# Optimization experiments

Measured on AMD Instinct MI355X. Metric: run time of the kernel, lower is better.

Reference implementation:

```python
import jax, jax.numpy as jnp
import numpy as np

B, D_IN, H1, H2, LAT, K = 32768, 512, 256, 128, 64, 2048
BN_EPS = 1e-5
COMMIT = 0.25


def _linear_w(k, i, o):
    # xavier-uniform-ish init
    lim = np.sqrt(6.0 / (i + o)).astype(np.float32)
    return jax.random.uniform(k, (i, o), jnp.float32, -lim, lim)


def _bn_params(keys, n):
    g = jax.random.uniform(keys[0], (n,), jnp.float32, 0.5, 1.5)
    b = 0.1 * jax.random.normal(keys[1], (n,), jnp.float32)
    m = 0.1 * jax.random.normal(keys[2], (n,), jnp.float32)
    v = jax.random.uniform(keys[3], (n,), jnp.float32, 0.5, 1.5)
    return g, b, m, v


def setup_inputs() -> dict:
    key = jax.random.key(0)
    ks = jax.random.split(key, 32)
    inp = {"x": jax.random.normal(ks[0], (B, D_IN), jnp.float32)}
    # encoder: 512 -> 256 -> 128 -> 64
    inp["ew1"], inp["eb1"] = _linear_w(ks[1], D_IN, H1), jnp.zeros((H1,), jnp.float32)
    inp["eg1"], inp["ebt1"], inp["em1"], inp["ev1"] = _bn_params(jax.random.split(ks[2], 4), H1)
    inp["ew2"], inp["eb2"] = _linear_w(ks[3], H1, H2), jnp.zeros((H2,), jnp.float32)
    inp["eg2"], inp["ebt2"], inp["em2"], inp["ev2"] = _bn_params(jax.random.split(ks[4], 4), H2)
    inp["ew3"], inp["eb3"] = _linear_w(ks[5], H2, LAT), jnp.zeros((LAT,), jnp.float32)
    # codebook (num_embeddings, latent_dim)
    inp["codebook"] = _linear_w(ks[6], K, LAT).reshape(K, LAT)
    # decoder: 64 -> 128 -> 256 -> 512
    inp["dw1"], inp["db1"] = _linear_w(ks[7], LAT, H2), jnp.zeros((H2,), jnp.float32)
    inp["dg1"], inp["dbt1"], inp["dm1"], inp["dv1"] = _bn_params(jax.random.split(ks[8], 4), H2)
    inp["dw2"], inp["db2"] = _linear_w(ks[9], H2, H1), jnp.zeros((H1,), jnp.float32)
    inp["dg2"], inp["dbt2"], inp["dm2"], inp["dv2"] = _bn_params(jax.random.split(ks[10], 4), H1)
    inp["dw3"], inp["db3"] = _linear_w(ks[11], H1, D_IN), jnp.zeros((D_IN,), jnp.float32)
    return inp


def _bn(x, g, b, m, v):
    # BatchNorm1d in eval mode: running stats
    return (x - m) * (g * jax.lax.rsqrt(v + BN_EPS)) + b


def reference(x, ew1, eb1, eg1, ebt1, em1, ev1,
              ew2, eb2, eg2, ebt2, em2, ev2,
              ew3, eb3, codebook,
              dw1, db1, dg1, dbt1, dm1, dv1,
              dw2, db2, dg2, dbt2, dm2, dv2,
              dw3, db3):
    # ---- encoder MLP (Dropout is identity in eval) ----
    h = _bn(jax.nn.relu(x @ ew1 + eb1), eg1, ebt1, em1, ev1)
    h = _bn(jax.nn.relu(h @ ew2 + eb2), eg2, ebt2, em2, ev2)
    z_e = h @ ew3 + eb3  # [B, LAT]

    # ---- vector quantization: cdist + argmin + gather ----
    # squared L2 distance (argmin-equivalent to cdist p=2)
    d2 = (jnp.sum(z_e * z_e, axis=1, keepdims=True)
          + jnp.sum(codebook * codebook, axis=1)[None, :]
          - 2.0 * (z_e @ codebook.T))  # [B, K]
    idx = jnp.argmin(d2, axis=-1)  # [B]
    z_q = codebook[idx]  # gather, [B, LAT]

    codebook_loss = jnp.mean((z_q - jax.lax.stop_gradient(z_e)) ** 2)
    commit_loss = jnp.mean((z_e - jax.lax.stop_gradient(z_q)) ** 2)
    vq_loss = codebook_loss + COMMIT * commit_loss

    # straight-through estimator
    z_q = z_e + jax.lax.stop_gradient(z_q - z_e)

    # ---- decoder MLP ----
    h = _bn(jax.nn.relu(z_q @ dw1 + db1), dg1, dbt1, dm1, dv1)
    h = _bn(jax.nn.relu(h @ dw2 + db2), dg2, dbt2, dm2, dv2)
    x_recon = h @ dw3 + db3  # [B, D_IN]

    recon_err = jnp.mean((x_recon - x) ** 2)
    return x_recon, vq_loss, idx, recon_err
```

## Files before the change

kernel.cpp:

```cpp
#include <hip/hip_runtime.h>

#define B_ROWS 32768
#define D_IN   512
#define H1_N   256
#define H2_N   128
#define LAT_N  64
#define K_CB   2048

#define VQ_MARGIN 6.0e-3f

typedef __attribute__((ext_vector_type(8))) short s8v;
typedef __attribute__((ext_vector_type(4))) float f4v;

__device__ inline unsigned short f2bf(float f) {
    union { float f; unsigned u; } v; v.f = f;
    unsigned r = v.u + 0x7fffu + ((v.u >> 16) & 1u);
    return (unsigned short)(r >> 16);
}
__device__ inline float bf2f(unsigned short h) {
    union { unsigned u; float f; } v; v.u = ((unsigned)h) << 16;
    return v.f;
}

template <int MODE, int K, int CT, bool ASPLIT>
__global__ __launch_bounds__(256, 2) void mfma_gemm(
    const float* __restrict__ A_f32,
    const unsigned short* __restrict__ A_hi,
    const unsigned short* __restrict__ A_lo,
    const unsigned short* __restrict__ w_hi,
    const unsigned short* __restrict__ w_lo,
    const float* __restrict__ bias,
    const float* __restrict__ bn_g, const float* __restrict__ bn_b,
    const float* __restrict__ bn_m, const float* __restrict__ bn_v,
    unsigned short* __restrict__ out_hi, unsigned short* __restrict__ out_lo,
    float* __restrict__ out_f32,
    const float* __restrict__ xref, float* __restrict__ partials, int N)
{
    const int lane = threadIdx.x & 63;
    const int wv = threadIdx.x >> 6;
    const int wr = wv >> 1, wc = wv & 1;
    const int rbase = blockIdx.x * 128 + wr * 64;
    const int cbase = blockIdx.y * (32 * CT) + wc * (16 * CT);
    const int lr = lane & 15, lg = lane >> 4;

    f4v acc[4][CT];
#pragma unroll
    for (int rt = 0; rt < 4; ++rt)
#pragma unroll
        for (int ct = 0; ct < CT; ++ct)
            acc[rt][ct] = (f4v){0.f, 0.f, 0.f, 0.f};

    for (int ks = 0; ks < K / 32; ++ks) {
        s8v ah[4], al[4], bh[CT], bl[CT];
#pragma unroll
        for (int rt = 0; rt < 4; ++rt) {
            size_t off = (size_t)(rbase + rt * 16 + lr) * K + ks * 32 + lg * 8;
            if constexpr (ASPLIT) {
                const float* p = &A_f32[off];
                float4 v0 = *reinterpret_cast<const float4*>(p);
                float4 v1 = *reinterpret_cast<const float4*>(p + 4);
                float fv[8] = {v0.x, v0.y, v0.z, v0.w, v1.x, v1.y, v1.z, v1.w};
                unsigned uu[8], llv[8];
#pragma unroll
                for (int j = 0; j < 8; ++j) {
                    uu[j] = __float_as_uint(fv[j]);
                    float lo = fv[j] - __uint_as_float(uu[j] & 0xffff0000u);
                    llv[j] = __float_as_uint(lo);
                }
                union { s8v v; unsigned w[4]; } H, L;
#pragma unroll
                for (int m = 0; m < 4; ++m) {
                    H.w[m] = __builtin_amdgcn_perm(uu[2 * m + 1], uu[2 * m], 0x07060302u);
                    L.w[m] = __builtin_amdgcn_perm(llv[2 * m + 1], llv[2 * m], 0x07060302u);
                }
                ah[rt] = H.v;
                al[rt] = L.v;
            } else {
                ah[rt] = *reinterpret_cast<const s8v*>(&A_hi[off]);
                al[rt] = *reinterpret_cast<const s8v*>(&A_lo[off]);
            }
        }
#pragma unroll
        for (int ct = 0; ct < CT; ++ct) {
            size_t off = (size_t)(cbase + ct * 16 + lr) * K + ks * 32 + lg * 8;
            bh[ct] = *reinterpret_cast<const s8v*>(&w_hi[off]);
            bl[ct] = *reinterpret_cast<const s8v*>(&w_lo[off]);
        }
#pragma unroll
        for (int rt = 0; rt < 4; ++rt)
#pragma unroll
            for (int ct = 0; ct < CT; ++ct) {
                acc[rt][ct] = __builtin_amdgcn_mfma_f32_16x16x32_bf16(
                    ah[rt], bh[ct], acc[rt][ct], 0, 0, 0);
                acc[rt][ct] = __builtin_amdgcn_mfma_f32_16x16x32_bf16(
                    al[rt], bh[ct], acc[rt][ct], 0, 0, 0);
                acc[rt][ct] = __builtin_amdgcn_mfma_f32_16x16x32_bf16(
                    ah[rt], bl[ct], acc[rt][ct], 0, 0, 0);
            }
    }

    float sq = 0.f;
#pragma unroll
    for (int ct = 0; ct < CT; ++ct) {
        int col = cbase + ct * 16 + lr;
        float bi = bias[col];
        float sc = 0.f, sh = 0.f;
        if (MODE == 0) {
            float s = bn_g[col] * rsqrtf(bn_v[col] + 1e-5f);
            sc = s;
            sh = bn_b[col] - bn_m[col] * s;
        }
#pragma unroll
        for (int rt = 0; rt < 4; ++rt)
#pragma unroll
            for (int i = 0; i < 4; ++i) {
                int row = rbase + rt * 16 + lg * 4 + i;
                float v = acc[rt][ct][i] + bi;
                if (MODE == 0) v = fmaxf(v, 0.f) * sc + sh;
                if (MODE == 0 || MODE == 3) {
                    unsigned u = __float_as_uint(v);
                    out_hi[(size_t)row * N + col] = (unsigned short)(u >> 16);
                    out_lo[(size_t)row * N + col] =
                        f2bf(v - __uint_as_float(u & 0xffff0000u));
                }
                if (MODE == 2) {
                    float d = v - xref[(size_t)row * N + col];
                    sq = fmaf(d, d, sq);
                }
                if (MODE == 2 || MODE == 3)
                    out_f32[(size_t)row * N + col] = v;
            }
    }
    if (MODE == 2) {
        __shared__ float red[256];
        red[threadIdx.x] = sq;
        __syncthreads();
        for (int off = 128; off > 0; off >>= 1) {
            if (threadIdx.x < off) red[threadIdx.x] += red[threadIdx.x + off];
            __syncthreads();
        }
        if (threadIdx.x == 0)
            partials[blockIdx.y * gridDim.x + blockIdx.x] = red[0];
    }
}

__device__ inline void wprep_body(const float* __restrict__ w,
                                  unsigned short* __restrict__ w_hi,
                                  unsigned short* __restrict__ w_lo,
                                  int K, int N, int idx)
{
    if (idx >= N * K) return;
    int n = idx / K, k = idx - n * K;
    float f = w[(size_t)k * N + n];
    unsigned u = __float_as_uint(f);
    float lo = f - __uint_as_float(u & 0xffff0000u);
    w_hi[idx] = (unsigned short)(u >> 16);
    w_lo[idx] = f2bf(lo);
}

__global__ __launch_bounds__(256) void prep_all(
    const float* __restrict__ dw3, unsigned short* w3hi, unsigned short* w3lo,
    const float* __restrict__ dw2, unsigned short* w2hi, unsigned short* w2lo,
    const float* __restrict__ dw1, unsigned short* w1hi, unsigned short* w1lo,
    const float* __restrict__ ew1, unsigned short* e1hi, unsigned short* e1lo,
    const float* __restrict__ ew2, unsigned short* e2hi, unsigned short* e2lo,
    const float* __restrict__ ew3, unsigned short* e3hi, unsigned short* e3lo,
    const float* __restrict__ cb, unsigned short* cb_hi, unsigned short* cb_lo,
    float* __restrict__ cn, int* __restrict__ rcnt, float* __restrict__ repairp)
{
    int bid = blockIdx.x;
    int tid = threadIdx.x;
    if (bid < 512) {
        wprep_body(dw3, w3hi, w3lo, H1_N, D_IN, bid * 256 + tid);
    } else if (bid < 640) {
        wprep_body(dw2, w2hi, w2lo, H2_N, H1_N, (bid - 512) * 256 + tid);
    } else if (bid < 672) {
        wprep_body(dw1, w1hi, w1lo, LAT_N, H2_N, (bid - 640) * 256 + tid);
    } else if (bid < 1184) {
        wprep_body(ew1, e1hi, e1lo, D_IN, H1_N, (bid - 672) * 256 + tid);
    } else if (bid < 1312) {
        wprep_body(ew2, e2hi, e2lo, H1_N, H2_N, (bid - 1184) * 256 + tid);
    } else if (bid < 1344) {
        wprep_body(ew3, e3hi, e3lo, H2_N, LAT_N, (bid - 1312) * 256 + tid);
    } else {
        int blk = bid - 1344;
        if (blk == 0) {
            if (tid == 0) rcnt[0] = 0;
            repairp[tid] = 0.f;
        }
        int j = blk * 256 + tid;
        float s = 0.f;
#pragma unroll
        for (int lq = 0; lq < 16; ++lq) {
            float4 v = *reinterpret_cast<const float4*>(&cb[(size_t)j * LAT_N + lq * 4]);
            float e[4] = {v.x, v.y, v.z, v.w};
            ushort4 h, l;
            unsigned short* hp = &h.x;
            unsigned short* lp = &l.x;
#pragma unroll
            for (int t = 0; t < 4; ++t) {
                s = fmaf(e[t], e[t], s);
                unsigned short hb = f2bf(e[t]);
                hp[t] = hb;
                lp[t] = f2bf(e[t] - bf2f(hb));
            }
            *reinterpret_cast<ushort4*>(&cb_hi[(size_t)j * LAT_N + lq * 4]) = h;
            *reinterpret_cast<ushort4*>(&cb_lo[(size_t)j * LAT_N + lq * 4]) = l;
        }
        cn[j] = s;
    }
}

__global__ __launch_bounds__(256) void vq_mfma(
    const unsigned short* __restrict__ zhi, const unsigned short* __restrict__ zlo,
    const unsigned short* __restrict__ cb_hi,
    const unsigned short* __restrict__ cb_lo, const float* __restrict__ cnorm,
    float4* __restrict__ cand)
{
    const int lane = threadIdx.x & 63;
    const int wid  = blockIdx.x * 4 + (threadIdx.x >> 6);
    const int rbase = (wid >> 3) * 64;
    const int cblk  = wid & 7;
    const int cbase = cblk * 256;
    const int lr = lane & 15;
    const int lg = lane >> 4;

    s8v a_hi[4][2], a_lo[4][2];
#pragma unroll
    for (int rt = 0; rt < 4; ++rt) {
        int row = rbase + rt * 16 + lr;
#pragma unroll
        for (int ks = 0; ks < 2; ++ks) {
            size_t off = (size_t)row * LAT_N + ks * 32 + lg * 8;
            a_hi[rt][ks] = *reinterpret_cast<const s8v*>(&zhi[off]);
            a_lo[rt][ks] = *reinterpret_cast<const s8v*>(&zlo[off]);
        }
    }

    float b1[4][4], b2[4][4];
    int j1[4][4];
#pragma unroll
    for (int rt = 0; rt < 4; ++rt)
#pragma unroll
        for (int i = 0; i < 4; ++i) {
            b1[rt][i] = 3.4e38f; b2[rt][i] = 3.4e38f; j1[rt][i] = 0;
        }

    for (int ct = 0; ct < 16; ++ct) {
        int col = cbase + ct * 16 + lr;
        const unsigned short* ph = &cb_hi[(size_t)col * LAT_N + lg * 8];
        const unsigned short* pl = &cb_lo[(size_t)col * LAT_N + lg * 8];
        s8v bh0 = *reinterpret_cast<const s8v*>(ph);
        s8v bh1 = *reinterpret_cast<const s8v*>(ph + 32);
        s8v bl0 = *reinterpret_cast<const s8v*>(pl);
        s8v bl1 = *reinterpret_cast<const s8v*>(pl + 32);
        float cn = cnorm[col];
#pragma unroll
        for (int rt = 0; rt < 4; ++rt) {
            f4v acc = {0.f, 0.f, 0.f, 0.f};
            acc = __builtin_amdgcn_mfma_f32_16x16x32_bf16(a_hi[rt][0], bh0, acc, 0, 0, 0);
            acc = __builtin_amdgcn_mfma_f32_16x16x32_bf16(a_hi[rt][1], bh1, acc, 0, 0, 0);
            acc = __builtin_amdgcn_mfma_f32_16x16x32_bf16(a_lo[rt][0], bh0, acc, 0, 0, 0);
            acc = __builtin_amdgcn_mfma_f32_16x16x32_bf16(a_lo[rt][1], bh1, acc, 0, 0, 0);
            acc = __builtin_amdgcn_mfma_f32_16x16x32_bf16(a_hi[rt][0], bl0, acc, 0, 0, 0);
            acc = __builtin_amdgcn_mfma_f32_16x16x32_bf16(a_hi[rt][1], bl1, acc, 0, 0, 0);
#pragma unroll
            for (int i = 0; i < 4; ++i) {
                float d = fmaf(-2.f, acc[i], cn);
                if (d < b1[rt][i]) {
                    b2[rt][i] = b1[rt][i];
                    b1[rt][i] = d;
                    j1[rt][i] = col;
                } else if (d < b2[rt][i]) {
                    b2[rt][i] = d;
                }
            }
        }
    }

#pragma unroll
    for (int off = 1; off < 16; off <<= 1) {
#pragma unroll
        for (int rt = 0; rt < 4; ++rt)
#pragma unroll
            for (int i = 0; i < 4; ++i) {
                float o1 = __shfl_xor(b1[rt][i], off);
                float o2 = __shfl_xor(b2[rt][i], off);
                int oj = __shfl_xor(j1[rt][i], off);
                float nb2 = fminf(fmaxf(b1[rt][i], o1), fminf(b2[rt][i], o2));
                if (o1 < b1[rt][i] ||
                    (o1 == b1[rt][i] && oj < j1[rt][i])) {
                    b1[rt][i] = o1;
                    j1[rt][i] = oj;
                }
                b2[rt][i] = nb2;
            }
    }
    if (lr == 0) {
#pragma unroll
        for (int rt = 0; rt < 4; ++rt)
#pragma unroll
            for (int i = 0; i < 4; ++i) {
                int row = rbase + rt * 16 + lg * 4 + i;
                cand[(size_t)row * 8 + cblk] = make_float4(
                    b1[rt][i], __int_as_float(j1[rt][i]), b2[rt][i], 0.f);
            }
    }
}

__global__ __launch_bounds__(256) void vq_merge(
    const float4* __restrict__ cand, const float* __restrict__ z,
    const float* __restrict__ cb,
    const unsigned short* __restrict__ cbhi,
    const unsigned short* __restrict__ cblo,
    unsigned short* __restrict__ zqhi, unsigned short* __restrict__ zqlo,
    float* __restrict__ idxf,
    int* __restrict__ rlist, int* __restrict__ rcnt,
    float* __restrict__ mergep)
{
    __shared__ float red[256];
    int tid = threadIdx.x;
    int row = blockIdx.x * 256 + tid;
    const float4* c = &cand[(size_t)row * 8];
    float4 c0 = c[0];
    float b1 = c0.x, b2 = c0.z;
    int j1 = __float_as_int(c0.y);
#pragma unroll
    for (int t = 1; t < 8; ++t) {
        float4 ct = c[t];
        float o1 = ct.x, o2 = ct.z;
        int oj = __float_as_int(ct.y);
        float nb2 = fminf(fmaxf(b1, o1), fminf(b2, o2));
        if (o1 < b1 || (o1 == b1 && oj < j1)) { b1 = o1; j1 = oj; }
        b2 = nb2;
    }
    idxf[row] = (float)j1;
    float sq = 0.f;
    if (b2 - b1 >= VQ_MARGIN) {
#pragma unroll
        for (int lq = 0; lq < 16; ++lq) {
            float4 cv = *reinterpret_cast<const float4*>(&cb[(size_t)j1 * LAT_N + lq * 4]);
            float4 zv = *reinterpret_cast<const float4*>(&z[(size_t)row * LAT_N + lq * 4]);
            float d0 = cv.x - zv.x, d1 = cv.y - zv.y;
            float d2 = cv.z - zv.z, d3 = cv.w - zv.w;
            sq = fmaf(d0, d0, sq); sq = fmaf(d1, d1, sq);
            sq = fmaf(d2, d2, sq); sq = fmaf(d3, d3, sq);
        }
        const uint4* gh = reinterpret_cast<const uint4*>(&cbhi[(size_t)j1 * LAT_N]);
        const uint4* gl = reinterpret_cast<const uint4*>(&cblo[(size_t)j1 * LAT_N]);
        uint4* dh = reinterpret_cast<uint4*>(&zqhi[(size_t)row * LAT_N]);
        uint4* dl = reinterpret_cast<uint4*>(&zqlo[(size_t)row * LAT_N]);
#pragma unroll
        for (int q = 0; q < 8; ++q) { dh[q] = gh[q]; dl[q] = gl[q]; }
    } else {
        int s = atomicAdd(rcnt, 1);
        if (s < B_ROWS) rlist[s] = row;
    }
    red[tid] = sq;
    __syncthreads();
    for (int off = 128; off > 0; off >>= 1) {
        if (tid < off) red[tid] += red[tid + off];
        __syncthreads();
    }
    if (tid == 0) mergep[blockIdx.x] = red[0];
}

#define RB 8
__global__ __launch_bounds__(256) void vq_repair(
    const int* __restrict__ rcnt, const int* __restrict__ rlist,
    const float* __restrict__ x,
    const float* __restrict__ ew1, const float* __restrict__ eb1,
    const float* __restrict__ eg1, const float* __restrict__ ebt1,
    const float* __restrict__ em1, const float* __restrict__ ev1,
    const float* __restrict__ ew2, const float* __restrict__ eb2,
    const float* __restrict__ eg2, const float* __restrict__ ebt2,
    const float* __restrict__ em2, const float* __restrict__ ev2,
    const float* __restrict__ ew3, const float* __restrict__ eb3,
    const float* __restrict__ cb, const float* __restrict__ cn,
    const unsigned short* __restrict__ cbhi,
    const unsigned short* __restrict__ cblo,
    unsigned short* __restrict__ zqhi, unsigned short* __restrict__ zqlo,
    float* __restrict__ idxf, float* __restrict__ repairp)
{
    __shared__ float sx[RB][D_IN];
    __shared__ float sh1[RB][H1_N];
    __shared__ float sh2[RB][H2_N];
    __shared__ float sz[RB][LAT_N];
    __shared__ float rv[256];
    __shared__ int ri[256];
    const int tid = threadIdx.x;
    const int count = min(rcnt[0], B_ROWS);
    if (blockIdx.x * RB >= count) return;
    float lsum = 0.f;
    for (int base = blockIdx.x * RB; base < count; base += gridDim.x * RB) {
        int nr = min(RB, count - base);
        __syncthreads();
        for (int s = tid; s < nr * (D_IN / 4); s += 256) {
            int r = s / (D_IN / 4), q = s - r * (D_IN / 4);
            int rr = rlist[base + r];
            rr = ((unsigned)rr < (unsigned)B_ROWS) ? rr : 0;
            *reinterpret_cast<float4*>(&sx[r][q * 4]) =
                *reinterpret_cast<const float4*>(&x[(size_t)rr * D_IN + q * 4]);
        }
        __syncthreads();
        {
            float a[RB];
#pragma unroll
            for (int r = 0; r < RB; ++r) a[r] = 0.f;
            for (int k = 0; k < D_IN; ++k) {
                float w = ew1[(size_t)k * H1_N + tid];
#pragma unroll
                for (int r = 0; r < RB; ++r) a[r] = fmaf(sx[r][k], w, a[r]);
            }
            float s1 = eg1[tid] * rsqrtf(ev1[tid] + 1e-5f);
            float t1 = ebt1[tid] - em1[tid] * s1;
            float bv = eb1[tid];
#pragma unroll
            for (int r = 0; r < RB; ++r) {
                float h = fmaxf(a[r] + bv, 0.f);
                sh1[r][tid] = h * s1 + t1;
            }
        }
        __syncthreads();
        {
            int c = tid & 127, rg = (tid >> 7) * 4;
            float a[4] = {0.f, 0.f, 0.f, 0.f};
            for (int k = 0; k < H1_N; ++k) {
                float w = ew2[(size_t)k * H2_N + c];
#pragma unroll
                for (int r = 0; r < 4; ++r) a[r] = fmaf(sh1[rg + r][k], w, a[r]);
            }
            float s2 = eg2[c] * rsqrtf(ev2[c] + 1e-5f);
            float t2 = ebt2[c] - em2[c] * s2;
            float bv = eb2[c];
#pragma unroll
            for (int r = 0; r < 4; ++r) {
                float h = fmaxf(a[r] + bv, 0.f);
                sh2[rg + r][c] = h * s2 + t2;
            }
        }
        __syncthreads();
        {
            int c = tid & 63, rg = (tid >> 6) * 2;
            float a0 = 0.f, a1 = 0.f;
            for (int k = 0; k < H2_N; ++k) {
                float w = ew3[(size_t)k * LAT_N + c];
                a0 = fmaf(sh2[rg][k], w, a0);
                a1 = fmaf(sh2[rg + 1][k], w, a1);
            }
            sz[rg][c] = a0 + eb3[c];
            sz[rg + 1][c] = a1 + eb3[c];
        }
        __syncthreads();
        float bv[RB];
        int bj[RB];
#pragma unroll
        for (int r = 0; r < RB; ++r) { bv[r] = 3.4e38f; bj[r] = 0; }
        for (int k = 0; k < K_CB / 256; ++k) {
            int cidx = tid + k * 256;
            float a[RB];
#pragma unroll
            for (int r = 0; r < RB; ++r) a[r] = 0.f;
            const float* cp = &cb[(size_t)cidx * LAT_N];
#pragma unroll 2
            for (int d4 = 0; d4 < 16; ++d4) {
                float4 cv = *reinterpret_cast<const float4*>(cp + d4 * 4);
#pragma unroll
                for (int r = 0; r < RB; ++r) {
                    a[r] = fmaf(sz[r][d4 * 4 + 0], cv.x, a[r]);
                    a[r] = fmaf(sz[r][d4 * 4 + 1], cv.y, a[r]);
                    a[r] = fmaf(sz[r][d4 * 4 + 2], cv.z, a[r]);
                    a[r] = fmaf(sz[r][d4 * 4 + 3], cv.w, a[r]);
                }
            }
            float cnv = cn[cidx];
#pragma unroll
            for (int r = 0; r < RB; ++r) {
                float d = fmaf(-2.f, a[r], cnv);
                if (d < bv[r] || (d == bv[r] && cidx < bj[r])) {
                    bv[r] = d; bj[r] = cidx;
                }
            }
        }
        for (int r = 0; r < RB; ++r) {
            if (r >= nr) break;
            rv[tid] = bv[r];
            ri[tid] = bj[r];
            __syncthreads();
            for (int off = 128; off > 0; off >>= 1) {
                if (tid < off) {
                    float ov = rv[tid + off];
                    int oi = ri[tid + off];
                    if (ov < rv[tid] || (ov == rv[tid] && oi < ri[tid])) {
                        rv[tid] = ov; ri[tid] = oi;
                    }
                }
                __syncthreads();
            }
            int bjf = ri[0];
            int rr = rlist[base + r];
            bool ok = (unsigned)rr < (unsigned)B_ROWS;
            rr = ok ? rr : 0;
            if (tid == 0 && ok) idxf[rr] = (float)bjf;
            float v = 0.f;
            if (tid < 64) {
                float d = cb[(size_t)bjf * LAT_N + tid] - sz[r][tid];
                v = d * d;
            }
            __syncthreads();
            rv[tid] = v;
            __syncthreads();
            for (int off = 128; off > 0; off >>= 1) {
                if (tid < off) rv[tid] += rv[tid + off];
                __syncthreads();
            }
            if (tid == 0) lsum += rv[0];
            if (ok) {
                if (tid < 8)
                    reinterpret_cast<uint4*>(&zqhi[(size_t)rr * LAT_N])[tid] =
                        reinterpret_cast<const uint4*>(&cbhi[(size_t)bjf * LAT_N])[tid];
                else if (tid < 16)
                    reinterpret_cast<uint4*>(&zqlo[(size_t)rr * LAT_N])[tid - 8] =
                        reinterpret_cast<const uint4*>(&cblo[(size_t)bjf * LAT_N])[tid - 8];
            }
            __syncthreads();
        }
    }
    if (tid == 0) repairp[blockIdx.x] = lsum;
}

__global__ __launch_bounds__(256) void finalize_kernel(
    const float* __restrict__ mergep, int nm,
    const float* __restrict__ repairp, int nr,
    const float* __restrict__ rep, int nre,
    float* __restrict__ vq_out, float* __restrict__ re_out)
{
    __shared__ float s[256];
    int tid = threadIdx.x;
    float a = 0.f;
    for (int i = tid; i < nm; i += 256) a += mergep[i];
    for (int i = tid; i < nr; i += 256) a += repairp[i];
    s[tid] = a;
    __syncthreads();
    for (int off = 128; off > 0; off >>= 1) {
        if (tid < off) s[tid] += s[tid + off];
        __syncthreads();
    }
    if (tid == 0) *vq_out = 1.25f * s[0] / (float)(B_ROWS * LAT_N);
    __syncthreads();
    float b = 0.f;
    for (int i = tid; i < nre; i += 256) b += rep[i];
    s[tid] = b;
    __syncthreads();
    for (int off = 128; off > 0; off >>= 1) {
        if (tid < off) s[tid] += s[tid + off];
        __syncthreads();
    }
    if (tid == 0) *re_out = s[0] / (float)(B_ROWS * D_IN);
}

extern "C" void kernel_launch(void* const* d_in, const int* in_sizes, int n_in,
                              void* d_out, int out_size, void* d_ws, size_t ws_size,
                              hipStream_t stream)
{
    const float* x    = (const float*)d_in[0];
    const float* ew1  = (const float*)d_in[1];
    const float* eb1  = (const float*)d_in[2];
    const float* eg1  = (const float*)d_in[3];
    const float* ebt1 = (const float*)d_in[4];
    const float* em1  = (const float*)d_in[5];
    const float* ev1  = (const float*)d_in[6];
    const float* ew2  = (const float*)d_in[7];
    const float* eb2  = (const float*)d_in[8];
    const float* eg2  = (const float*)d_in[9];
    const float* ebt2 = (const float*)d_in[10];
    const float* em2  = (const float*)d_in[11];
    const float* ev2  = (const float*)d_in[12];
    const float* ew3  = (const float*)d_in[13];
    const float* eb3  = (const float*)d_in[14];
    const float* cb   = (const float*)d_in[15];
    const float* dw1  = (const float*)d_in[16];
    const float* db1  = (const float*)d_in[17];
    const float* dg1  = (const float*)d_in[18];
    const float* dbt1 = (const float*)d_in[19];
    const float* dm1  = (const float*)d_in[20];
    const float* dv1  = (const float*)d_in[21];
    const float* dw2  = (const float*)d_in[22];
    const float* db2  = (const float*)d_in[23];
    const float* dg2  = (const float*)d_in[24];
    const float* dbt2 = (const float*)d_in[25];
    const float* dm2  = (const float*)d_in[26];
    const float* dv2  = (const float*)d_in[27];
    const float* dw3  = (const float*)d_in[28];
    const float* db3  = (const float*)d_in[29];

    float* outf = (float*)d_out;
    const size_t XR_OFF = 0;
    const size_t VQ_OFF = (size_t)B_ROWS * D_IN;
    const size_t IDX_OFF = VQ_OFF + 1;
    const size_t RE_OFF = IDX_OFF + B_ROWS;

    float* wsf = (float*)d_ws;
    size_t off = 0;
    float* buf256 = wsf + off; off += (size_t)B_ROWS * H1_N;
    float* buf128 = wsf + off; off += (size_t)B_ROWS * H2_N;
    float* zbuf   = wsf + off; off += (size_t)B_ROWS * LAT_N;
    float* cnbuf  = wsf + off; off += K_CB;
    float* mergep = wsf + off; off += 128;
    float* repairp= wsf + off; off += 256;
    float* rep    = wsf + off; off += 1024;
    unsigned short* cbhi = (unsigned short*)(wsf + off); off += K_CB * LAT_N / 2;
    unsigned short* cblo = (unsigned short*)(wsf + off); off += K_CB * LAT_N / 2;
    float4* candb = (float4*)(wsf + off); off += (size_t)B_ROWS * 8 * 4;
    int* rcnt  = (int*)(wsf + off); off += 16;
    int* rlist = (int*)(wsf + off); off += B_ROWS;
    unsigned short* w1hi = (unsigned short*)(wsf + off); off += (H2_N * LAT_N) / 2;
    unsigned short* w1lo = (unsigned short*)(wsf + off); off += (H2_N * LAT_N) / 2;
    unsigned short* w2hi = (unsigned short*)(wsf + off); off += (H1_N * H2_N) / 2;
    unsigned short* w2lo = (unsigned short*)(wsf + off); off += (H1_N * H2_N) / 2;
    unsigned short* w3hi = (unsigned short*)(wsf + off); off += (D_IN * H1_N) / 2;
    unsigned short* w3lo = (unsigned short*)(wsf + off); off += (D_IN * H1_N) / 2;
    unsigned short* e1hi = (unsigned short*)(wsf + off); off += (D_IN * H1_N) / 2;
    unsigned short* e1lo = (unsigned short*)(wsf + off); off += (D_IN * H1_N) / 2;
    unsigned short* e2hi = (unsigned short*)(wsf + off); off += (H1_N * H2_N) / 2;
    unsigned short* e2lo = (unsigned short*)(wsf + off); off += (H1_N * H2_N) / 2;
    unsigned short* e3hi = (unsigned short*)(wsf + off); off += (H2_N * LAT_N) / 2;
    unsigned short* e3lo = (unsigned short*)(wsf + off); off += (H2_N * LAT_N) / 2;
    unsigned short* zqhi = (unsigned short*)(wsf + off); off += (size_t)B_ROWS * LAT_N / 2;
    unsigned short* zqlo = (unsigned short*)(wsf + off); off += (size_t)B_ROWS * LAT_N / 2;

    unsigned short* eh1hi = (unsigned short*)buf256;
    unsigned short* eh1lo = (unsigned short*)(buf256 + (size_t)B_ROWS * 128);
    unsigned short* zhi   = (unsigned short*)buf256;
    unsigned short* zlo   = (unsigned short*)(buf256 + (size_t)B_ROWS * 32);
    unsigned short* dh2hi = (unsigned short*)buf256;
    unsigned short* dh2lo = (unsigned short*)(buf256 + (size_t)B_ROWS * 128);
    unsigned short* eh2hi = (unsigned short*)buf128;
    unsigned short* eh2lo = (unsigned short*)(buf128 + (size_t)B_ROWS * 64);
    unsigned short* dh1hi = (unsigned short*)buf128;
    unsigned short* dh1lo = (unsigned short*)(buf128 + (size_t)B_ROWS * 64);

    dim3 blk(256);
    const int GXM = B_ROWS / 128;

    prep_all<<<dim3(1352), blk, 0, stream>>>(
        dw3, w3hi, w3lo, dw2, w2hi, w2lo, dw1, w1hi, w1lo,
        ew1, e1hi, e1lo, ew2, e2hi, e2lo, ew3, e3hi, e3lo,
        cb, cbhi, cblo, cnbuf, rcnt, repairp);

    mfma_gemm<0, D_IN, 4, true><<<dim3(GXM, H1_N / 128), blk, 0, stream>>>(
        x, nullptr, nullptr, e1hi, e1lo, eb1, eg1, ebt1, em1, ev1,
        eh1hi, eh1lo, nullptr, nullptr, nullptr, H1_N);
    mfma_gemm<0, H1_N, 4, false><<<dim3(GXM, 1), blk, 0, stream>>>(
        nullptr, eh1hi, eh1lo, e2hi, e2lo, eb2, eg2, ebt2, em2, ev2,
        eh2hi, eh2lo, nullptr, nullptr, nullptr, H2_N);
    mfma_gemm<3, H2_N, 2, false><<<dim3(GXM, 1), blk, 0, stream>>>(
        nullptr, eh2hi, eh2lo, e3hi, e3lo, eb3, nullptr, nullptr, nullptr, nullptr,
        zhi, zlo, zbuf, nullptr, nullptr, LAT_N);

    vq_mfma<<<dim3(1024), blk, 0, stream>>>(zhi, zlo, cbhi, cblo, cnbuf, candb);
    vq_merge<<<dim3(B_ROWS / 256), blk, 0, stream>>>(
        candb, zbuf, cb, cbhi, cblo, zqhi, zqlo,
        outf + IDX_OFF, rlist, rcnt, mergep);
    vq_repair<<<dim3(256), blk, 0, stream>>>(
        rcnt, rlist, x,
        ew1, eb1, eg1, ebt1, em1, ev1,
        ew2, eb2, eg2, ebt2, em2, ev2,
        ew3, eb3, cb, cnbuf, cbhi, cblo, zqhi, zqlo,
        outf + IDX_OFF, repairp);

    mfma_gemm<0, LAT_N, 4, false><<<dim3(GXM, 1), blk, 0, stream>>>(
        nullptr, zqhi, zqlo, w1hi, w1lo, db1, dg1, dbt1, dm1, dv1,
        dh1hi, dh1lo, nullptr, nullptr, nullptr, H2_N);
    mfma_gemm<0, H2_N, 4, false><<<dim3(GXM, H1_N / 128), blk, 0, stream>>>(
        nullptr, dh1hi, dh1lo, w2hi, w2lo, db2, dg2, dbt2, dm2, dv2,
        dh2hi, dh2lo, nullptr, nullptr, nullptr, H1_N);
    mfma_gemm<2, H1_N, 4, false><<<dim3(GXM, D_IN / 128), blk, 0, stream>>>(
        nullptr, dh2hi, dh2lo, w3hi, w3lo, db3, nullptr, nullptr, nullptr, nullptr,
        nullptr, nullptr, outf + XR_OFF, x, rep, D_IN);

    finalize_kernel<<<dim3(1), blk, 0, stream>>>(
        mergep, 128, repairp, 256, rep, 1024, outf + VQ_OFF, outf + RE_OFF);
}
```

Baseline: 501.9 us.

## Split VQ repair encoder recompute into tiled fp32 GEMM kernels over gathered rows

The fp32 re-encoding of ambiguous VQ rows moves out of the single repair kernel, which handled 8 rows per block with weights read straight from global memory. It now runs as three register- and shared-memory-tiled fp32 GEMM kernels (64-row tiles, swizzled A tile) over the gathered row list, writing z to a new buffer. A slimmer repair_scan kernel then does only the codebook search. The aim is much better weight reuse and parallelism when many rows need repair. The cost is extra launches, a large grid of mostly early-exiting blocks, and extra intermediate memory traffic.

```diff
diff --git a/kernel.cpp b/kernel.cpp
--- a/kernel.cpp
+++ b/kernel.cpp
@@ -8,6 +8,8 @@
 #define K_CB   2048
 
 #define VQ_MARGIN 6.0e-3f
+#define BK 32
+#define BN 128
 
 typedef __attribute__((ext_vector_type(8))) short s8v;
 typedef __attribute__((ext_vector_type(4))) float f4v;
@@ -21,6 +23,8 @@
     union { unsigned u; float f; } v; v.u = ((unsigned)h) << 16;
     return v.f;
 }
+
+#define SWZ(row) ((((row) >> 2) & 7) << 3)
 
 template <int MODE, int K, int CT, bool ASPLIT>
 __global__ __launch_bounds__(256, 2) void mfma_gemm(
@@ -141,6 +145,125 @@
         }
         if (threadIdx.x == 0)
             partials[blockIdx.y * gridDim.x + blockIdx.x] = red[0];
+    }
+}
+
+template <int MODE, bool GATHER>
+__global__ __launch_bounds__(256, 6) void rgemm(
+    const int* __restrict__ rcnt, const int* __restrict__ rlist,
+    const float* __restrict__ A, const float* __restrict__ W,
+    const float* __restrict__ bias,
+    const float* __restrict__ bn_g, const float* __restrict__ bn_b,
+    const float* __restrict__ bn_m, const float* __restrict__ bn_v,
+    float* __restrict__ out, int M, int N)
+{
+    const int count = min(rcnt[0], B_ROWS);
+    const int row0 = blockIdx.x * 64;
+    if (row0 >= count) return;
+    __shared__ float sA[BK][64];
+    __shared__ float sB[BK][BN];
+    const int tid = threadIdx.x;
+    const int tr = tid >> 4;
+    const int tc = tid & 15;
+    const int n0 = blockIdx.y * BN;
+
+    float acc[4][8];
+#pragma unroll
+    for (int i = 0; i < 4; ++i)
+#pragma unroll
+        for (int j = 0; j < 8; ++j) acc[i][j] = 0.f;
+
+    for (int k0 = 0; k0 < M; k0 += BK) {
+#pragma unroll
+        for (int it = 0; it < 2; ++it) {
+            int s = tid + it * 256;
+            int m = s >> 3;
+            int kq = s & 7;
+            int i = row0 + m;
+            int src;
+            if (GATHER) {
+                int rr = (i < count) ? rlist[i] : 0;
+                src = ((unsigned)rr < (unsigned)B_ROWS) ? rr : 0;
+            } else {
+                src = i;
+            }
+            float4 v = *reinterpret_cast<const float4*>(
+                &A[(size_t)src * M + k0 + kq * 4]);
+            int kk = kq * 4;
+            sA[kk + 0][m ^ SWZ(kk + 0)] = v.x;
+            sA[kk + 1][m ^ SWZ(kk + 1)] = v.y;
+            sA[kk + 2][m ^ SWZ(kk + 2)] = v.z;
+            sA[kk + 3][m ^ SWZ(kk + 3)] = v.w;
+        }
+#pragma unroll
+        for (int it = 0; it < 4; ++it) {
+            int s = tid + it * 256;
+            int k = s >> 5;
+            int nq = s & 31;
+            int n = n0 + nq * 4;
+            float4 v = make_float4(0.f, 0.f, 0.f, 0.f);
+            if (n < N)
+                v = *reinterpret_cast<const float4*>(&W[(size_t)(k0 + k) * N + n]);
+            *reinterpret_cast<float4*>(&sB[k][nq * 4]) = v;
+        }
+        __syncthreads();
+#pragma unroll 4
+        for (int k = 0; k < BK; ++k) {
+            int ac = (tr * 4) ^ SWZ(k);
+            float4 a0 = *reinterpret_cast<float4*>(&sA[k][ac]);
+            float a[4] = {a0.x, a0.y, a0.z, a0.w};
+            float4 b0 = *reinterpret_cast<float4*>(&sB[k][tc * 4]);
+            float4 b1 = *reinterpret_cast<float4*>(&sB[k][64 + tc * 4]);
+            float b[8] = {b0.x, b0.y, b0.z, b0.w, b1.x, b1.y, b1.z, b1.w};
+#pragma unroll
+            for (int i = 0; i < 4; ++i)
+#pragma unroll
+                for (int j = 0; j < 8; ++j)
+                    acc[i][j] = fmaf(a[i], b[j], acc[i][j]);
+        }
+        __syncthreads();
+    }
+
+    const int nb0 = n0 + tc * 4;
+    const int nb1 = n0 + 64 + tc * 4;
+    float bi[8], sc[8], sh[8];
+#pragma unroll
+    for (int g = 0; g < 2; ++g) {
+        int nb = g ? nb1 : nb0;
+        if (nb < N) {
+#pragma unroll
+            for (int j = 0; j < 4; ++j) {
+                int n = nb + j;
+                bi[g * 4 + j] = bias[n];
+                if (MODE == 0) {
+                    float s = bn_g[n] * rsqrtf(bn_v[n] + 1e-5f);
+                    sc[g * 4 + j] = s;
+                    sh[g * 4 + j] = bn_b[n] - bn_m[n] * s;
+                }
+            }
+        }
+    }
+#pragma unroll
+    for (int i = 0; i < 4; ++i) {
+        int row = row0 + tr * 4 + i;
+#pragma unroll
+        for (int g = 0; g < 2; ++g) {
+            int nb = g ? nb1 : nb0;
+            if (nb < N) {
+                float o[4];
+#pragma unroll
+                for (int j = 0; j < 4; ++j) {
+                    float v = acc[i][g * 4 + j] + bi[g * 4 + j];
+                    if (MODE == 0) {
+                        v = v > 0.f ? v : 0.f;
+                        v = v * sc[g * 4 + j] + sh[g * 4 + j];
+                    }
+                    o[j] = v;
+                }
+                *reinterpret_cast<float4*>(&out[(size_t)row * N + nb]) =
+                    make_float4(o[0], o[1], o[2], o[3]);
+            }
+        }
     }
 }
 
@@ -366,25 +489,15 @@
 }
 
 #define RB 8
-__global__ __launch_bounds__(256) void vq_repair(
+__global__ __launch_bounds__(256) void repair_scan(
     const int* __restrict__ rcnt, const int* __restrict__ rlist,
-    const float* __restrict__ x,
-    const float* __restrict__ ew1, const float* __restrict__ eb1,
-    const float* __restrict__ eg1, const float* __restrict__ ebt1,
-    const float* __restrict__ em1, const float* __restrict__ ev1,
-    const float* __restrict__ ew2, const float* __restrict__ eb2,
-    const float* __restrict__ eg2, const float* __restrict__ ebt2,
-    const float* __restrict__ em2, const float* __restrict__ ev2,
-    const float* __restrict__ ew3, const float* __restrict__ eb3,
+    const float* __restrict__ zr,
     const float* __restrict__ cb, const float* __restrict__ cn,
     const unsigned short* __restrict__ cbhi,
     const unsigned short* __restrict__ cblo,
     unsigned short* __restrict__ zqhi, unsigned short* __restrict__ zqlo,
     float* __restrict__ idxf, float* __restrict__ repairp)
 {
-    __shared__ float sx[RB][D_IN];
-    __shared__ float sh1[RB][H1_N];
-    __shared__ float sh2[RB][H2_N];
     __shared__ float sz[RB][LAT_N];
     __shared__ float rv[256];
     __shared__ int ri[256];
@@ -395,61 +508,9 @@
     for (int base = blockIdx.x * RB; base < count; base += gridDim.x * RB) {
         int nr = min(RB, count - base);
         __syncthreads();
-        for (int s = tid; s < nr * (D_IN / 4); s += 256) {
-            int r = s / (D_IN / 4), q = s - r * (D_IN / 4);
-            int rr = rlist[base + r];
-            rr = ((unsigned)rr < (unsigned)B_ROWS) ? rr : 0;
-            *reinterpret_cast<float4*>(&sx[r][q * 4]) =
-                *reinterpret_cast<const float4*>(&x[(size_t)rr * D_IN + q * 4]);
-        }
-        __syncthreads();
-        {
-            float a[RB];
-#pragma unroll
-            for (int r = 0; r < RB; ++r) a[r] = 0.f;
-            for (int k = 0; k < D_IN; ++k) {
-                float w = ew1[(size_t)k * H1_N + tid];
-#pragma unroll
-                for (int r = 0; r < RB; ++r) a[r] = fmaf(sx[r][k], w, a[r]);
-            }
-            float s1 = eg1[tid] * rsqrtf(ev1[tid] + 1e-5f);
-            float t1 = ebt1[tid] - em1[tid] * s1;
-            float bv = eb1[tid];
-#pragma unroll
-            for (int r = 0; r < RB; ++r) {
-                float h = fmaxf(a[r] + bv, 0.f);
-                sh1[r][tid] = h * s1 + t1;
-            }
-        }
-        __syncthreads();
-        {
-            int c = tid & 127, rg = (tid >> 7) * 4;
-            float a[4] = {0.f, 0.f, 0.f, 0.f};
-            for (int k = 0; k < H1_N; ++k) {
-                float w = ew2[(size_t)k * H2_N + c];
-#pragma unroll
-                for (int r = 0; r < 4; ++r) a[r] = fmaf(sh1[rg + r][k], w, a[r]);
-            }
-            float s2 = eg2[c] * rsqrtf(ev2[c] + 1e-5f);
-            float t2 = ebt2[c] - em2[c] * s2;
-            float bv = eb2[c];
-#pragma unroll
-            for (int r = 0; r < 4; ++r) {
-                float h = fmaxf(a[r] + bv, 0.f);
-                sh2[rg + r][c] = h * s2 + t2;
-            }
-        }
-        __syncthreads();
-        {
-            int c = tid & 63, rg = (tid >> 6) * 2;
-            float a0 = 0.f, a1 = 0.f;
-            for (int k = 0; k < H2_N; ++k) {
-                float w = ew3[(size_t)k * LAT_N + c];
-                a0 = fmaf(sh2[rg][k], w, a0);
-                a1 = fmaf(sh2[rg + 1][k], w, a1);
-            }
-            sz[rg][c] = a0 + eb3[c];
-            sz[rg + 1][c] = a1 + eb3[c];
+        for (int s = tid; s < nr * LAT_N; s += 256) {
+            int r = s >> 6, d = s & 63;
+            sz[r][d] = zr[(size_t)(base + r) * LAT_N + d];
         }
         __syncthreads();
         float bv[RB];
@@ -605,6 +666,7 @@
     float* buf256 = wsf + off; off += (size_t)B_ROWS * H1_N;
     float* buf128 = wsf + off; off += (size_t)B_ROWS * H2_N;
     float* zbuf   = wsf + off; off += (size_t)B_ROWS * LAT_N;
+    float* zr     = wsf + off; off += (size_t)B_ROWS * LAT_N;
     float* cnbuf  = wsf + off; off += K_CB;
     float* mergep = wsf + off; off += 128;
     float* repairp= wsf + off; off += 256;
@@ -633,10 +695,12 @@
     unsigned short* eh1lo = (unsigned short*)(buf256 + (size_t)B_ROWS * 128);
     unsigned short* zhi   = (unsigned short*)buf256;
     unsigned short* zlo   = (unsigned short*)(buf256 + (size_t)B_ROWS * 32);
+    float*          h1r   = buf256;
     unsigned short* dh2hi = (unsigned short*)buf256;
     unsigned short* dh2lo = (unsigned short*)(buf256 + (size_t)B_ROWS * 128);
     unsigned short* eh2hi = (unsigned short*)buf128;
     unsigned short* eh2lo = (unsigned short*)(buf128 + (size_t)B_ROWS * 64);
+    float*          h2r   = buf128;
     unsigned short* dh1hi = (unsigned short*)buf128;
     unsigned short* dh1lo = (unsigned short*)(buf128 + (size_t)B_ROWS * 64);
 
@@ -662,11 +726,16 @@
     vq_merge<<<dim3(B_ROWS / 256), blk, 0, stream>>>(
         candb, zbuf, cb, cbhi, cblo, zqhi, zqlo,
         outf + IDX_OFF, rlist, rcnt, mergep);
-    vq_repair<<<dim3(256), blk, 0, stream>>>(
-        rcnt, rlist, x,
-        ew1, eb1, eg1, ebt1, em1, ev1,
-        ew2, eb2, eg2, ebt2, em2, ev2,
-        ew3, eb3, cb, cnbuf, cbhi, cblo, zqhi, zqlo,
+
+    rgemm<0, true><<<dim3(B_ROWS / 64, 2), blk, 0, stream>>>(
+        rcnt, rlist, x, ew1, eb1, eg1, ebt1, em1, ev1, h1r, D_IN, H1_N);
+    rgemm<0, false><<<dim3(B_ROWS / 64, 1), blk, 0, stream>>>(
+        rcnt, rlist, h1r, ew2, eb2, eg2, ebt2, em2, ev2, h2r, H1_N, H2_N);
+    rgemm<1, false><<<dim3(B_ROWS / 64, 1), blk, 0, stream>>>(
+        rcnt, rlist, h2r, ew3, eb3, nullptr, nullptr, nullptr, nullptr,
+        zr, H2_N, LAT_N);
+    repair_scan<<<dim3(256), blk, 0, stream>>>(
+        rcnt, rlist, zr, cb, cnbuf, cbhi, cblo, zqhi, zqlo,
         outf + IDX_OFF, repairp);
 
     mfma_gemm<0, LAT_N, 4, false><<<dim3(GXM, 1), blk, 0, stream>>>(
```

Measured after the change: 479.3 us. 4.5% less time.
